# Performance work log

Hardware: AMD Instinct MI355X
Metric: run time of the kernel (lower is better)

Reference implementation:

```python
import jax, jax.numpy as jnp
import numpy as np

B, S, D = 4, 2048, 512
H, DQK, DV = 6, 64, 64
PROJ = (DQK + DQK + DV) * H  # 1152
EPS = 1e-5


def setup_inputs() -> dict:
    key = jax.random.key(0)
    ks = jax.random.split(key, 5)
    sc = 0.05
    return {
        "x": jax.random.normal(ks[0], (B, S, D), jnp.float32),
        "Wp": jax.random.normal(ks[1], (PROJ, D), jnp.float32) * sc,
        "bp": jax.random.normal(ks[2], (PROJ,), jnp.float32) * sc,
        "Wo": jax.random.normal(ks[3], (D, H * DV), jnp.float32) * sc,
        "bo": jax.random.normal(ks[4], (D,), jnp.float32) * sc,
        "gamma": jnp.ones((D,), jnp.float32),
        "beta": jnp.zeros((D,), jnp.float32),
    }


def reference(x, Wp, bp, Wo, bo, gamma, beta):
    b, s, d = x.shape
    # 1x1 Conv1d projection == pointwise linear: [b,s,d] @ [d,proj] -> [b,s,proj]
    proj = jnp.einsum("bsd,pd->bsp", x, Wp) + bp
    q, k, v = proj[..., : H * DQK], proj[..., H * DQK : 2 * H * DQK], proj[..., 2 * H * DQK :]
    # split heads -> [b,h,s,depth]
    q = q.reshape(b, s, H, DQK).transpose(0, 2, 1, 3)
    k = k.reshape(b, s, H, DQK).transpose(0, 2, 1, 3)
    v = v.reshape(b, s, H, DV).transpose(0, 2, 1, 3)
    scores = jnp.einsum("bhqd,bhkd->bhqk", q, k) / jnp.sqrt(jnp.float32(DQK))
    attn = jax.nn.softmax(scores, axis=-1)  # softmax over kv axis
    out = jnp.einsum("bhqk,bhkd->bhqd", attn, v)
    # concat heads -> [b,s,h*dv]
    concat = out.transpose(0, 2, 1, 3).reshape(b, s, H * DV)
    y = jnp.einsum("bsf,df->bsd", concat, Wo) + bo
    z = x + y
    mu = jnp.mean(z, axis=-1, keepdims=True)
    var = jnp.mean(jnp.square(z - mu), axis=-1, keepdims=True)
    return (z - mu) / jnp.sqrt(var + EPS) * gamma + beta
```

## Files before the change

kernel.cpp:

```cpp
#include <hip/hip_runtime.h>

typedef __bf16 bf16;
typedef __bf16 bf16x8 __attribute__((ext_vector_type(8)));
typedef __bf16 bf16x4 __attribute__((ext_vector_type(4)));
typedef float  f32x4  __attribute__((ext_vector_type(4)));

#define BB 4
#define SS 2048
#define DD 512
#define HH 6
#define DH 64
#define PROJ 1152
#define FF 384
#define LDK 72

__device__ __forceinline__ bool probe_fp32(const unsigned* p) {
    return p[0] == 0x3F800000u;
}

__device__ __forceinline__ void async16(const bf16* g, bf16* l) {
    __builtin_amdgcn_global_load_lds(
        (const __attribute__((address_space(1))) void*)g,
        (__attribute__((address_space(3))) void*)l, 16, 0, 0);
}

struct CvtSrcs { const void* s[7]; };

#define CB0 524288
#define CB1 598016
#define CB2 622592
#define CB3 622736
#define CB4 622800
#define CB5 622864
#define CB6 622928

__global__ __launch_bounds__(256) void cvt_all_kernel(
    CvtSrcs srcs, bf16* __restrict__ dst, const unsigned* __restrict__ probe)
{
    const int t = blockIdx.x * 256 + threadIdx.x;
    if (t >= CB6) return;
    int seg, base;
    if      (t < CB0) { seg = 0; base = 0;   }
    else if (t < CB1) { seg = 1; base = CB0; }
    else if (t < CB2) { seg = 2; base = CB1; }
    else if (t < CB3) { seg = 3; base = CB2; }
    else if (t < CB4) { seg = 4; base = CB3; }
    else if (t < CB5) { seg = 5; base = CB4; }
    else              { seg = 6; base = CB5; }
    const int li = (t - base) * 8;
    if (probe_fp32(probe)) {
        const float* s = (const float*)srcs.s[seg] + li;
        bf16x8 o;
#pragma unroll
        for (int j = 0; j < 8; ++j) o[j] = (bf16)s[j];
        *(bf16x8*)&dst[(size_t)t * 8] = o;
    } else {
        *(bf16x8*)&dst[(size_t)t * 8] =
            *(const bf16x8*)((const bf16*)srcs.s[seg] + li);
    }
}

__global__ __launch_bounds__(256) void gemm_bt_kernel(
    const bf16* __restrict__ A, const bf16* __restrict__ B,
    const bf16* __restrict__ bias, void* __restrict__ Cout,
    int M, int N, int K, int store_f32)
{
    __shared__ __attribute__((aligned(16))) bf16 sA[8192];
    __shared__ __attribute__((aligned(16))) bf16 sB[8192];

    const int tid  = threadIdx.x;
    const int lane = tid & 63;
    const int wave = tid >> 6;
    const int wmb = (wave >> 1) * 4;
    const int wnb = (wave & 1) * 4;
    const int l15 = lane & 15;
    const int quad = lane >> 4;
    const int bm = blockIdx.x * 128;
    const int bn = blockIdx.y * 128;

    const bf16* pA[4];
    const bf16* pB[4];
#pragma unroll
    for (int j = 0; j < 4; ++j) {
        int c = wave * 4 + j;
        int row = (c >> 1) * 16 + (lane & 15);
        int col = ((c & 1) << 5) + (lane >> 4) * 8;
        pA[j] = A + (size_t)(bm + row) * K + col;
        pB[j] = B + (size_t)(bn + row) * K + col;
    }

    const f32x4 fzero = {0.f, 0.f, 0.f, 0.f};
    f32x4 acc[4][4];
#pragma unroll
    for (int mi = 0; mi < 4; ++mi)
#pragma unroll
        for (int ni = 0; ni < 4; ++ni) acc[mi][ni] = fzero;

    for (int k0 = 0; k0 < K; k0 += 64) {
        __syncthreads();
#pragma unroll
        for (int j = 0; j < 4; ++j) {
            int c = wave * 4 + j;
            async16(pA[j], &sA[c * 512]);
            async16(pB[j], &sB[c * 512]);
            pA[j] += 64;
            pB[j] += 64;
        }
        __syncthreads();

#pragma unroll
        for (int kk = 0; kk < 2; ++kk) {
            bf16x8 af[4], bfr[4];
#pragma unroll
            for (int i = 0; i < 4; ++i) {
                af[i]  = *(const bf16x8*)&sA[((wmb + i) * 128 + kk * 64 + quad * 16 + l15) * 8];
                bfr[i] = *(const bf16x8*)&sB[((wnb + i) * 128 + kk * 64 + quad * 16 + l15) * 8];
            }
#pragma unroll
            for (int mi = 0; mi < 4; ++mi)
#pragma unroll
                for (int ni = 0; ni < 4; ++ni)
                    acc[mi][ni] = __builtin_amdgcn_mfma_f32_16x16x32_bf16(
                        af[mi], bfr[ni], acc[mi][ni], 0, 0, 0);
        }
    }

#pragma unroll
    for (int mi = 0; mi < 4; ++mi) {
        int row = bm + (wmb + mi) * 16 + quad * 4;
#pragma unroll
        for (int ni = 0; ni < 4; ++ni) {
            int col = bn + (wnb + ni) * 16 + l15;
            float bv = (float)bias[col];
#pragma unroll
            for (int r = 0; r < 4; ++r) {
                float v = acc[mi][ni][r] + bv;
                if (store_f32) ((float*)Cout)[(size_t)(row + r) * N + col] = v;
                else           ((bf16*)Cout)[(size_t)(row + r) * N + col] = (bf16)v;
            }
        }
    }
}

__global__ __launch_bounds__(256) void vt_kernel(
    const bf16* __restrict__ proj, bf16* __restrict__ Vt)
{
    __shared__ __attribute__((aligned(16))) bf16 lt[64 * LDK];

    const int tid = threadIdx.x;
    const int s0 = blockIdx.x * 64;
    const int bh = blockIdx.y;
    const int b = bh / HH, h = bh % HH;

#pragma unroll
    for (int i = 0; i < 2; ++i) {
        int vid = i * 256 + tid;
        int sl = vid >> 3;
        int dc = (vid & 7) << 3;
        bf16x8 v = *(const bf16x8*)&proj[
            (size_t)(b * SS + s0 + sl) * PROJ + 2 * HH * DH + h * DH + dc];
#pragma unroll
        for (int j = 0; j < 8; ++j) {
            int d = dc + j;
            lt[d * LDK + (sl ^ (((d >> 3) & 3) * 8))] = v[j];
        }
    }
    __syncthreads();

#pragma unroll
    for (int i = 0; i < 2; ++i) {
        int vid = i * 256 + tid;
        int d = vid >> 3;
        int sc = (vid & 7) << 3;
        bf16x8 v = *(const bf16x8*)&lt[d * LDK + (sc ^ (((d >> 3) & 3) * 8))];
        *(bf16x8*)&Vt[(size_t)bh * DH * SS + (size_t)d * SS + s0 + sc] = v;
    }
}

__global__ __launch_bounds__(256) void attn_kernel(
    const bf16* __restrict__ proj, const bf16* __restrict__ Vt,
    bf16* __restrict__ Opart, float* __restrict__ lpart)
{
    __shared__ __attribute__((aligned(16))) bf16 sK [64 * LDK];
    __shared__ __attribute__((aligned(16))) bf16 sVt[64 * LDK];
    __shared__ __attribute__((aligned(16))) bf16 sP [4 * 32 * LDK];

    const int tid  = threadIdx.x;
    const int lane = tid & 63;
    const int wave = tid >> 6;
    const int l15  = lane & 15;
    const int quad = lane >> 4;

    const int bh = blockIdx.y;
    const int b = bh / HH, h = bh % HH;
    const int q0 = blockIdx.x * 128;
    const int kz = blockIdx.z;
    const bf16* base = proj + (size_t)b * SS * PROJ;
    const bf16* vtb  = Vt + (size_t)bh * DH * SS;

    const int sr = tid >> 3;
    const int sc = (tid & 7) << 3;

    bf16x8 qf[2][2];
#pragma unroll
    for (int g = 0; g < 2; ++g) {
        const int qrow = q0 + wave * 32 + g * 16 + l15;
#pragma unroll
        for (int ks = 0; ks < 2; ++ks) {
            qf[ks][g] = *(const bf16x8*)&base[
                (size_t)qrow * PROJ + h * DH + ks * 32 + quad * 8];
#pragma unroll
            for (int j = 0; j < 8; ++j)
                qf[ks][g][j] = (bf16)((float)qf[ks][g][j] * 0.125f);
        }
    }

    const f32x4 fzero = {0.f, 0.f, 0.f, 0.f};
    float l_part[2] = {0.f, 0.f};
    f32x4 oacc[2][4];
#pragma unroll
    for (int g = 0; g < 2; ++g)
#pragma unroll
        for (int fi = 0; fi < 4; ++fi) oacc[g][fi] = fzero;

    bf16* pw = &sP[wave * 32 * LDK];

    const int kt0 = kz * (SS / 128);
    const int kt1 = kt0 + SS / 128;

    bf16x8 kreg[2], vreg[2];
#pragma unroll
    for (int i = 0; i < 2; ++i) {
        int r = i * 32 + sr;
        kreg[i] = *(const bf16x8*)&base[(size_t)(kt0 * 64 + r) * PROJ + HH * DH + h * DH + sc];
        vreg[i] = *(const bf16x8*)&vtb[(size_t)r * SS + kt0 * 64 + sc];
    }

    for (int kt = kt0; kt < kt1; ++kt) {
        __syncthreads();
#pragma unroll
        for (int i = 0; i < 2; ++i) {
            int r = i * 32 + sr;
            *(bf16x8*)&sK [r * LDK + sc] = kreg[i];
            *(bf16x8*)&sVt[r * LDK + sc] = vreg[i];
        }
        __syncthreads();
        if (kt + 1 < kt1) {
#pragma unroll
            for (int i = 0; i < 2; ++i) {
                int r = i * 32 + sr;
                kreg[i] = *(const bf16x8*)&base[
                    (size_t)((kt + 1) * 64 + r) * PROJ + HH * DH + h * DH + sc];
                vreg[i] = *(const bf16x8*)&vtb[(size_t)r * SS + (kt + 1) * 64 + sc];
            }
        }

        f32x4 st[2][4];
#pragma unroll
        for (int g = 0; g < 2; ++g)
#pragma unroll
            for (int mi = 0; mi < 4; ++mi) st[g][mi] = fzero;
#pragma unroll
        for (int ks = 0; ks < 2; ++ks)
#pragma unroll
            for (int mi = 0; mi < 4; ++mi) {
                bf16x8 af = *(const bf16x8*)&sK[(mi * 16 + l15) * LDK + ks * 32 + quad * 8];
#pragma unroll
                for (int g = 0; g < 2; ++g)
                    st[g][mi] = __builtin_amdgcn_mfma_f32_16x16x32_bf16(
                        af, qf[ks][g], st[g][mi], 0, 0, 0);
            }

#pragma unroll
        for (int g = 0; g < 2; ++g)
#pragma unroll
            for (int mi = 0; mi < 4; ++mi)
#pragma unroll
                for (int r = 0; r < 4; ++r) {
                    st[g][mi][r] = __expf(st[g][mi][r]);
                    l_part[g] += st[g][mi][r];
                }

#pragma unroll
        for (int g = 0; g < 2; ++g)
#pragma unroll
            for (int mi = 0; mi < 4; ++mi) {
                bf16x4 p4;
#pragma unroll
                for (int r = 0; r < 4; ++r) p4[r] = (bf16)st[g][mi][r];
                *(bf16x4*)&pw[(g * 16 + l15) * LDK + mi * 16 + quad * 4] = p4;
            }

#pragma unroll
        for (int ks = 0; ks < 2; ++ks) {
            bf16x8 bfrag[2];
#pragma unroll
            for (int g = 0; g < 2; ++g)
                bfrag[g] = *(const bf16x8*)&pw[(g * 16 + l15) * LDK + ks * 32 + quad * 8];
#pragma unroll
            for (int fi = 0; fi < 4; ++fi) {
                bf16x8 af = *(const bf16x8*)&sVt[(fi * 16 + l15) * LDK + ks * 32 + quad * 8];
#pragma unroll
                for (int g = 0; g < 2; ++g)
                    oacc[g][fi] = __builtin_amdgcn_mfma_f32_16x16x32_bf16(
                        af, bfrag[g], oacc[g][fi], 0, 0, 0);
            }
        }
    }

#pragma unroll
    for (int g = 0; g < 2; ++g) {
        l_part[g] += __shfl_xor(l_part[g], 16);
        l_part[g] += __shfl_xor(l_part[g], 32);
    }

    const size_t zoff = (size_t)(kz * BB * HH + bh) * SS;
#pragma unroll
    for (int g = 0; g < 2; ++g) {
        const int qg = q0 + wave * 32 + g * 16 + l15;
        bf16* orow = Opart + (zoff + qg) * DH;
#pragma unroll
        for (int fi = 0; fi < 4; ++fi) {
            bf16x4 o4;
#pragma unroll
            for (int r = 0; r < 4; ++r) o4[r] = (bf16)oacc[g][fi][r];
            *(bf16x4*)&orow[fi * 16 + quad * 4] = o4;
        }
    }
    if (lane < 16) {
#pragma unroll
        for (int g = 0; g < 2; ++g)
            lpart[zoff + q0 + wave * 32 + g * 16 + lane] = l_part[g];
    }
}

__global__ __launch_bounds__(256) void attn_merge_kernel(
    const bf16* __restrict__ Opart, const float* __restrict__ lpart,
    bf16* __restrict__ concat)
{
    const int g = blockIdx.x * 256 + threadIdx.x;
    const int d8 = g & 7;
    const int q  = (g >> 3) & (SS - 1);
    const int bh = g >> 14;
    const int b = bh / HH, h = bh % HH;

    const size_t off0 = ((size_t)bh * SS + q) * DH + d8 * 8;
    const size_t off1 = ((size_t)(BB * HH + bh) * SS + q) * DH + d8 * 8;
    bf16x8 a0 = *(const bf16x8*)&Opart[off0];
    bf16x8 a1 = *(const bf16x8*)&Opart[off1];
    float invl = 1.f / (lpart[(size_t)bh * SS + q] +
                        lpart[(size_t)(BB * HH + bh) * SS + q]);
    bf16x8 o;
#pragma unroll
    for (int j = 0; j < 8; ++j)
        o[j] = (bf16)(((float)a0[j] + (float)a1[j]) * invl);
    *(bf16x8*)&concat[((size_t)(b * SS + q)) * FF + h * DH + d8 * 8] = o;
}

__global__ __launch_bounds__(256) void ln_kernel(
    const void* __restrict__ xr, const float* __restrict__ y,
    const bf16* __restrict__ gamma, const bf16* __restrict__ beta,
    void* __restrict__ out, const unsigned* __restrict__ probe)
{
    const bool f32 = probe_fp32(probe);
    const int lane = threadIdx.x & 63;
    const int wave = threadIdx.x >> 6;
    const int row = blockIdx.x * 4 + wave;
    const size_t off = (size_t)row * DD + lane * 8;

    float z[8];
    if (f32) {
        const float* xf = (const float*)xr;
#pragma unroll
        for (int j = 0; j < 8; ++j) z[j] = xf[off + j];
    } else {
        bf16x8 xv = *(const bf16x8*)&((const bf16*)xr)[off];
#pragma unroll
        for (int j = 0; j < 8; ++j) z[j] = (float)xv[j];
    }
    f32x4 y0 = *(const f32x4*)&y[off];
    f32x4 y1 = *(const f32x4*)&y[off + 4];
#pragma unroll
    for (int j = 0; j < 4; ++j) { z[j] += y0[j]; z[j + 4] += y1[j]; }

    float s = 0.f;
#pragma unroll
    for (int j = 0; j < 8; ++j) s += z[j];
#pragma unroll
    for (int m = 1; m < 64; m <<= 1) s += __shfl_xor(s, m);
    float mu = s * (1.f / DD);
    float s2 = 0.f;
#pragma unroll
    for (int j = 0; j < 8; ++j) { float d = z[j] - mu; s2 += d * d; }
#pragma unroll
    for (int m = 1; m < 64; m <<= 1) s2 += __shfl_xor(s2, m);
    float rs = rsqrtf(s2 * (1.f / DD) + 1e-5f);

    bf16x8 gm = *(const bf16x8*)&gamma[lane * 8];
    bf16x8 be = *(const bf16x8*)&beta[lane * 8];
    if (f32) {
        f32x4 o0, o1;
#pragma unroll
        for (int j = 0; j < 4; ++j) {
            o0[j] = (z[j]     - mu) * rs * (float)gm[j]     + (float)be[j];
            o1[j] = (z[j + 4] - mu) * rs * (float)gm[j + 4] + (float)be[j + 4];
        }
        *(f32x4*)&((float*)out)[off]     = o0;
        *(f32x4*)&((float*)out)[off + 4] = o1;
    } else {
        bf16x8 o;
#pragma unroll
        for (int j = 0; j < 8; ++j)
            o[j] = (bf16)((z[j] - mu) * rs * (float)gm[j] + (float)be[j]);
        *(bf16x8*)&((bf16*)out)[off] = o;
    }
}

extern "C" void kernel_launch(void* const* d_in, const int* in_sizes, int n_in,
                              void* d_out, int out_size, void* d_ws, size_t ws_size,
                              hipStream_t stream)
{
    const unsigned* probe = (const unsigned*)d_in[5];

    char* ws = (char*)d_ws;
    size_t o = 0;
    bf16* xb   = (bf16*)(ws + o); o += (size_t)BB * SS * DD * 2;
    bf16* Wpb  = (bf16*)(ws + o); o += (size_t)PROJ * DD * 2;
    bf16* Wob  = (bf16*)(ws + o); o += (size_t)DD * FF * 2;
    bf16* bpb  = (bf16*)(ws + o); o += PROJ * 2;
    bf16* bob  = (bf16*)(ws + o); o += DD * 2;
    bf16* gb   = (bf16*)(ws + o); o += DD * 2;
    bf16* bb   = (bf16*)(ws + o); o += DD * 2;
    bf16* proj = (bf16*)(ws + o); o += (size_t)BB * SS * PROJ * 2;
    bf16* concat = (bf16*)(ws + o); o += (size_t)BB * SS * FF * 2;
    bf16* vtbuf  = (bf16*)(ws + o); o += (size_t)BB * HH * DH * SS * 2;
    bf16* Opart  = (bf16*)(ws + o); o += (size_t)2 * BB * HH * SS * DH * 2;
    float* lpart = (float*)(ws + o); o += (size_t)2 * BB * HH * SS * 4;
    float* ybuf = (float*)proj;

    CvtSrcs srcs;
    srcs.s[0] = d_in[0]; srcs.s[1] = d_in[1]; srcs.s[2] = d_in[3];
    srcs.s[3] = d_in[2]; srcs.s[4] = d_in[4]; srcs.s[5] = d_in[5];
    srcs.s[6] = d_in[6];
    cvt_all_kernel<<<(CB6 + 255) / 256, 256, 0, stream>>>(srcs, xb, probe);

    gemm_bt_kernel<<<dim3((BB * SS) / 128, PROJ / 128), 256, 0, stream>>>(
        xb, Wpb, bpb, proj, BB * SS, PROJ, DD, 0);
    vt_kernel<<<dim3(SS / 64, BB * HH), 256, 0, stream>>>(proj, vtbuf);
    attn_kernel<<<dim3(SS / 128, BB * HH, 2), 256, 0, stream>>>(
        proj, vtbuf, Opart, lpart);
    attn_merge_kernel<<<(BB * HH * SS * 8) / 256, 256, 0, stream>>>(
        Opart, lpart, concat);
    gemm_bt_kernel<<<dim3((BB * SS) / 128, DD / 128), 256, 0, stream>>>(
        concat, Wob, bob, ybuf, BB * SS, DD, FF, 1);
    ln_kernel<<<dim3((BB * SS) / 4), 256, 0, stream>>>(
        d_in[0], ybuf, gb, bb, d_out, probe);
}
```

Measured before the change: 189.6 us.

## Fuse attention split-merge into output projection GEMM A-tile loading

Removes the separate attn_merge kernel and the concat buffer. The output-projection GEMM now reads both split-K partial outputs and their softmax denominators directly, normalizes them in registers, and writes the merged tile to LDS. The GEMM load path also changes from async global-to-LDS copies to register-staged loads with padded LDS rows, prefetching the next K tile during compute. This saves one launch and a full round trip of the concat tensor through memory. In exchange, the A-operand loads become strided per head, and the QKV projection GEMM also switches to the register-staged path, which may behave differently from the async copies.

```diff
diff --git a/kernel.cpp b/kernel.cpp
--- a/kernel.cpp
+++ b/kernel.cpp
@@ -16,12 +16,6 @@
 
 __device__ __forceinline__ bool probe_fp32(const unsigned* p) {
     return p[0] == 0x3F800000u;
-}
-
-__device__ __forceinline__ void async16(const bf16* g, bf16* l) {
-    __builtin_amdgcn_global_load_lds(
-        (const __attribute__((address_space(1))) void*)g,
-        (__attribute__((address_space(3))) void*)l, 16, 0, 0);
 }
 
 struct CvtSrcs { const void* s[7]; };
@@ -60,33 +54,57 @@
     }
 }
 
+template<int MERGE, int STORE_F32>
 __global__ __launch_bounds__(256) void gemm_bt_kernel(
-    const bf16* __restrict__ A, const bf16* __restrict__ B,
-    const bf16* __restrict__ bias, void* __restrict__ Cout,
-    int M, int N, int K, int store_f32)
-{
-    __shared__ __attribute__((aligned(16))) bf16 sA[8192];
-    __shared__ __attribute__((aligned(16))) bf16 sB[8192];
+    const bf16* __restrict__ A, const float* __restrict__ lpart,
+    const bf16* __restrict__ B, const bf16* __restrict__ bias,
+    void* __restrict__ Cout, int M, int N, int K)
+{
+    __shared__ __attribute__((aligned(16))) bf16 sA[128 * LDK];
+    __shared__ __attribute__((aligned(16))) bf16 sB[128 * LDK];
 
     const int tid  = threadIdx.x;
     const int lane = tid & 63;
     const int wave = tid >> 6;
-    const int wmb = (wave >> 1) * 4;
-    const int wnb = (wave & 1) * 4;
+    const int wm = (wave >> 1) * 64;
+    const int wn = (wave & 1) * 64;
     const int l15 = lane & 15;
     const int quad = lane >> 4;
     const int bm = blockIdx.x * 128;
     const int bn = blockIdx.y * 128;
-
-    const bf16* pA[4];
-    const bf16* pB[4];
+    const int KT = K / 64;
+
+    int srow[4], scol;
+    scol = (tid & 7) << 3;
+#pragma unroll
+    for (int j = 0; j < 4; ++j) srow[j] = (j * 256 + tid) >> 3;
+
+    const bf16* pA[4]; const bf16* pB[4];
+    const float* pl0[4];
 #pragma unroll
     for (int j = 0; j < 4; ++j) {
-        int c = wave * 4 + j;
-        int row = (c >> 1) * 16 + (lane & 15);
-        int col = ((c & 1) << 5) + (lane >> 4) * 8;
-        pA[j] = A + (size_t)(bm + row) * K + col;
-        pB[j] = B + (size_t)(bn + row) * K + col;
+        if (MERGE) {
+            int row = bm + srow[j];
+            int b = row >> 11, q = row & (SS - 1);
+            pA[j]  = A + ((size_t)(b * HH) * SS + q) * DH + scol;
+            pl0[j] = lpart + (size_t)(b * HH) * SS + q;
+        } else {
+            pA[j] = A + (size_t)(bm + srow[j]) * K + scol;
+        }
+        pB[j] = B + (size_t)(bn + srow[j]) * K + scol;
+    }
+
+    bf16x8 ar0[4], ar1[4], br[4];
+    float li0[4], li1[4];
+#pragma unroll
+    for (int j = 0; j < 4; ++j) {
+        ar0[j] = *(const bf16x8*)pA[j];
+        if (MERGE) {
+            ar1[j] = *(const bf16x8*)(pA[j] + (size_t)BB * HH * SS * DH);
+            li0[j] = pl0[j][0];
+            li1[j] = pl0[j][(size_t)BB * HH * SS];
+        }
+        br[j] = *(const bf16x8*)pB[j];
     }
 
     const f32x4 fzero = {0.f, 0.f, 0.f, 0.f};
@@ -96,25 +114,50 @@
 #pragma unroll
         for (int ni = 0; ni < 4; ++ni) acc[mi][ni] = fzero;
 
-    for (int k0 = 0; k0 < K; k0 += 64) {
+    for (int kt = 0; kt < KT; ++kt) {
         __syncthreads();
 #pragma unroll
         for (int j = 0; j < 4; ++j) {
-            int c = wave * 4 + j;
-            async16(pA[j], &sA[c * 512]);
-            async16(pB[j], &sB[c * 512]);
-            pA[j] += 64;
-            pB[j] += 64;
+            if (MERGE) {
+                float inv = 1.f / (li0[j] + li1[j]);
+                bf16x8 m;
+#pragma unroll
+                for (int e = 0; e < 8; ++e)
+                    m[e] = (bf16)(((float)ar0[j][e] + (float)ar1[j][e]) * inv);
+                *(bf16x8*)&sA[srow[j] * LDK + scol] = m;
+            } else {
+                *(bf16x8*)&sA[srow[j] * LDK + scol] = ar0[j];
+            }
+            *(bf16x8*)&sB[srow[j] * LDK + scol] = br[j];
         }
         __syncthreads();
+
+        if (kt + 1 < KT) {
+#pragma unroll
+            for (int j = 0; j < 4; ++j) {
+                if (MERGE) {
+                    pA[j]  += (size_t)SS * DH;
+                    pl0[j] += SS;
+                    ar0[j] = *(const bf16x8*)pA[j];
+                    ar1[j] = *(const bf16x8*)(pA[j] + (size_t)BB * HH * SS * DH);
+                    li0[j] = pl0[j][0];
+                    li1[j] = pl0[j][(size_t)BB * HH * SS];
+                } else {
+                    pA[j] += 64;
+                    ar0[j] = *(const bf16x8*)pA[j];
+                }
+                pB[j] += 64;
+                br[j] = *(const bf16x8*)pB[j];
+            }
+        }
 
 #pragma unroll
         for (int kk = 0; kk < 2; ++kk) {
             bf16x8 af[4], bfr[4];
 #pragma unroll
             for (int i = 0; i < 4; ++i) {
-                af[i]  = *(const bf16x8*)&sA[((wmb + i) * 128 + kk * 64 + quad * 16 + l15) * 8];
-                bfr[i] = *(const bf16x8*)&sB[((wnb + i) * 128 + kk * 64 + quad * 16 + l15) * 8];
+                af[i]  = *(const bf16x8*)&sA[(wm + i * 16 + l15) * LDK + kk * 32 + quad * 8];
+                bfr[i] = *(const bf16x8*)&sB[(wn + i * 16 + l15) * LDK + kk * 32 + quad * 8];
             }
 #pragma unroll
             for (int mi = 0; mi < 4; ++mi)
@@ -127,15 +170,15 @@
 
 #pragma unroll
     for (int mi = 0; mi < 4; ++mi) {
-        int row = bm + (wmb + mi) * 16 + quad * 4;
+        int row = bm + wm + mi * 16 + quad * 4;
 #pragma unroll
         for (int ni = 0; ni < 4; ++ni) {
-            int col = bn + (wnb + ni) * 16 + l15;
+            int col = bn + wn + ni * 16 + l15;
             float bv = (float)bias[col];
 #pragma unroll
             for (int r = 0; r < 4; ++r) {
                 float v = acc[mi][ni][r] + bv;
-                if (store_f32) ((float*)Cout)[(size_t)(row + r) * N + col] = v;
+                if (STORE_F32) ((float*)Cout)[(size_t)(row + r) * N + col] = v;
                 else           ((bf16*)Cout)[(size_t)(row + r) * N + col] = (bf16)v;
             }
         }
@@ -332,29 +375,6 @@
         for (int g = 0; g < 2; ++g)
             lpart[zoff + q0 + wave * 32 + g * 16 + lane] = l_part[g];
     }
-}
-
-__global__ __launch_bounds__(256) void attn_merge_kernel(
-    const bf16* __restrict__ Opart, const float* __restrict__ lpart,
-    bf16* __restrict__ concat)
-{
-    const int g = blockIdx.x * 256 + threadIdx.x;
-    const int d8 = g & 7;
-    const int q  = (g >> 3) & (SS - 1);
-    const int bh = g >> 14;
-    const int b = bh / HH, h = bh % HH;
-
-    const size_t off0 = ((size_t)bh * SS + q) * DH + d8 * 8;
-    const size_t off1 = ((size_t)(BB * HH + bh) * SS + q) * DH + d8 * 8;
-    bf16x8 a0 = *(const bf16x8*)&Opart[off0];
-    bf16x8 a1 = *(const bf16x8*)&Opart[off1];
-    float invl = 1.f / (lpart[(size_t)bh * SS + q] +
-                        lpart[(size_t)(BB * HH + bh) * SS + q]);
-    bf16x8 o;
-#pragma unroll
-    for (int j = 0; j < 8; ++j)
-        o[j] = (bf16)(((float)a0[j] + (float)a1[j]) * invl);
-    *(bf16x8*)&concat[((size_t)(b * SS + q)) * FF + h * DH + d8 * 8] = o;
 }
 
 __global__ __launch_bounds__(256) void ln_kernel(
@@ -432,7 +452,6 @@
     bf16* gb   = (bf16*)(ws + o); o += DD * 2;
     bf16* bb   = (bf16*)(ws + o); o += DD * 2;
     bf16* proj = (bf16*)(ws + o); o += (size_t)BB * SS * PROJ * 2;
-    bf16* concat = (bf16*)(ws + o); o += (size_t)BB * SS * FF * 2;
     bf16* vtbuf  = (bf16*)(ws + o); o += (size_t)BB * HH * DH * SS * 2;
     bf16* Opart  = (bf16*)(ws + o); o += (size_t)2 * BB * HH * SS * DH * 2;
     float* lpart = (float*)(ws + o); o += (size_t)2 * BB * HH * SS * 4;
@@ -444,15 +463,13 @@
     srcs.s[6] = d_in[6];
     cvt_all_kernel<<<(CB6 + 255) / 256, 256, 0, stream>>>(srcs, xb, probe);
 
-    gemm_bt_kernel<<<dim3((BB * SS) / 128, PROJ / 128), 256, 0, stream>>>(
-        xb, Wpb, bpb, proj, BB * SS, PROJ, DD, 0);
+    gemm_bt_kernel<0, 0><<<dim3((BB * SS) / 128, PROJ / 128), 256, 0, stream>>>(
+        xb, nullptr, Wpb, bpb, proj, BB * SS, PROJ, DD);
     vt_kernel<<<dim3(SS / 64, BB * HH), 256, 0, stream>>>(proj, vtbuf);
     attn_kernel<<<dim3(SS / 128, BB * HH, 2), 256, 0, stream>>>(
         proj, vtbuf, Opart, lpart);
-    attn_merge_kernel<<<(BB * HH * SS * 8) / 256, 256, 0, stream>>>(
-        Opart, lpart, concat);
-    gemm_bt_kernel<<<dim3((BB * SS) / 128, DD / 128), 256, 0, stream>>>(
-        concat, Wob, bob, ybuf, BB * SS, DD, FF, 1);
+    gemm_bt_kernel<1, 1><<<dim3((BB * SS) / 128, DD / 128), 256, 0, stream>>>(
+        Opart, lpart, Wob, bob, ybuf, BB * SS, DD, FF);
     ln_kernel<<<dim3((BB * SS) / 4), 256, 0, stream>>>(
         d_in[0], ybuf, gb, bb, d_out, probe);
 }
```

Measured after the change: 166.7 us. -12.1%, faster.
